# Kernel optimization log

Measured on AMD Instinct MI355X. Metric: run time of the kernel, lower is better.

The kernel has to match this reference:

```python
import jax, jax.numpy as jnp
import numpy as np

N = 50000
E = 600000
F_IN = 128      # float features (in_channels - 1)
CE = 8          # cell embedding dim
D_IN = F_IN + CE  # 136
C = 128         # out_channels
NUM_CELLS = 854
NEG_SLOPE = 0.2
LN_EPS = 1e-5


def _gat_layer(x, src, dst, W, a_src, a_dst, b):
    """PyG GATConv, heads=1, concat=False, add_self_loops already in src/dst.
    x: [N, Din]; src/dst: [Etot]; W: [Din, C]; a_src/a_dst: [C]; b: [C].
    """
    h = x @ W                               # [N, C]
    alpha_src = h @ a_src                   # [N]
    alpha_dst = h @ a_dst                   # [N]
    e = jax.nn.leaky_relu(alpha_src[src] + alpha_dst[dst], NEG_SLOPE)  # [Etot]
    # segment softmax over edges sharing a destination node
    m = jax.ops.segment_max(e, dst, num_segments=N)    # [N] (every node has a self-loop)
    ex = jnp.exp(e - m[dst])                           # [Etot]
    denom = jax.ops.segment_sum(ex, dst, num_segments=N)  # [N]
    alpha = ex / denom[dst]                            # [Etot]
    out = jax.ops.segment_sum(h[src] * alpha[:, None], dst, num_segments=N)  # [N, C]
    return out + b


def _layer_norm(x, g, b):
    mu = jnp.mean(x, axis=-1, keepdims=True)
    var = jnp.var(x, axis=-1, keepdims=True)
    return (x - mu) * jax.lax.rsqrt(var + LN_EPS) * g + b


def setup_inputs() -> dict:
    key = jax.random.key(0)
    ks = jax.random.split(key, 12)
    x_base = jax.random.normal(ks[0], (N, F_IN), dtype=jnp.float32)
    cell_ids = jax.random.randint(ks[1], (N,), 0, NUM_CELLS, dtype=jnp.int64)
    edge_index = jax.random.randint(ks[2], (2, E), 0, N, dtype=jnp.int64)
    s = 0.05
    cell_emb = jax.random.normal(ks[3], (NUM_CELLS, CE), dtype=jnp.float32)
    W1 = jax.random.normal(ks[4], (D_IN, C), dtype=jnp.float32) * s
    a_src1 = jax.random.normal(ks[5], (C,), dtype=jnp.float32) * s
    a_dst1 = jax.random.normal(ks[6], (C,), dtype=jnp.float32) * s
    b1 = jnp.zeros((C,), dtype=jnp.float32)
    ln_g = jnp.ones((C,), dtype=jnp.float32)
    ln_b = jnp.zeros((C,), dtype=jnp.float32)
    W2 = jax.random.normal(ks[7], (C, C), dtype=jnp.float32) * s
    a_src2 = jax.random.normal(ks[8], (C,), dtype=jnp.float32) * s
    a_dst2 = jax.random.normal(ks[9], (C,), dtype=jnp.float32) * s
    b2 = jnp.zeros((C,), dtype=jnp.float32)
    return {
        "x_base": x_base, "cell_ids": cell_ids, "edge_index": edge_index,
        "cell_emb": cell_emb,
        "W1": W1, "a_src1": a_src1, "a_dst1": a_dst1, "b1": b1,
        "ln_g": ln_g, "ln_b": ln_b,
        "W2": W2, "a_src2": a_src2, "a_dst2": a_dst2, "b2": b2,
    }


def reference(x_base, cell_ids, edge_index, cell_emb,
              W1, a_src1, a_dst1, b1, ln_g, ln_b,
              W2, a_src2, a_dst2, b2):
    # embed cell ids and concat (equiv. to x[:, :-1] + Embedding(x[:, -1]))
    x = jnp.concatenate([x_base, cell_emb[cell_ids]], axis=1)   # [N, 136]
    # PyG GATConv adds self-loops internally
    loops = jnp.arange(N, dtype=edge_index.dtype)
    src = jnp.concatenate([edge_index[0], loops])
    dst = jnp.concatenate([edge_index[1], loops])
    # layer 1 + LN + ELU (dropout inactive in eval mode)
    x = _gat_layer(x, src, dst, W1, a_src1, a_dst1, b1)
    x = jax.nn.elu(_layer_norm(x, ln_g, ln_b))
    # layer 2 (no norm/activation on last layer)
    x = _gat_layer(x, src, dst, W2, a_src2, a_dst2, b2)
    return x
```

## Files before the change

### kernel.cpp

```cpp
#include <hip/hip_runtime.h>
#include <hip/hip_fp16.h>
#include <cstdint>
#include <cstddef>

#define NEG_SLOPE 0.2f
#define LN_EPS 1e-5f

constexpr int BS = 256;
constexpr int STRIDE = 96;

typedef _Float16 f16x8 __attribute__((ext_vector_type(8)));
typedef float f32x4 __attribute__((ext_vector_type(4)));

__global__ void k_build(
    const int* __restrict__ esrc, const int* __restrict__ edst,
    int* __restrict__ cnt, int* __restrict__ sn,
    const float* __restrict__ x, const int* __restrict__ cid,
    const float* __restrict__ emb, _Float16* __restrict__ xb,
    const float* __restrict__ W1, const float* __restrict__ W2,
    _Float16* __restrict__ Wt1, _Float16* __restrict__ Wt2,
    int e, int etot, int n, int npad, int nbE, int xblocks)
{
    int b = blockIdx.x;
    if (b < nbE) {
        int i = b * BS + threadIdx.x;
        if (i >= etot) return;
        int s, d;
        if (i < e) { s = esrc[i]; d = edst[i]; }
        else       { s = d = i - e; }
        int slot = atomicAdd(&cnt[d], 1);
        if (slot < STRIDE)
            sn[d * STRIDE + slot] = s << 8;
    } else if (b < nbE + xblocks) {
        int r = (b - nbE) * 8 + (threadIdx.x >> 5);
        int c = threadIdx.x & 31;
        if (r >= npad) return;
        _Float16* row = xb + (size_t)r * 160;
        if (r < n) {
            const float* xr = x + (size_t)r * 128;
            #pragma unroll
            for (int k = 0; k < 4; ++k) row[c + 32 * k] = (_Float16)xr[c + 32 * k];
            float v = (c < 8) ? emb[cid[r] * 8 + c] : 0.f;
            row[128 + c] = (_Float16)v;
        } else {
            #pragma unroll
            for (int k = 0; k < 5; ++k) row[c + 32 * k] = (_Float16)0.f;
        }
    } else {
        int idx = (b - nbE - xblocks) * BS + threadIdx.x;
        if (idx < 128 * 160) {
            int nn = idx / 160, k = idx - nn * 160;
            Wt1[idx] = (_Float16)((k < 136) ? W1[(size_t)k * 128 + nn] : 0.f);
        } else if (idx < 128 * 160 + 128 * 128) {
            int j = idx - 128 * 160;
            int nn = j >> 7, k = j & 127;
            Wt2[j] = (_Float16)W2[(size_t)k * 128 + nn];
        }
    }
}

template<int KP>
__global__ __launch_bounds__(64) void k_gemm_mfma(
    const _Float16* __restrict__ A, const _Float16* __restrict__ Bt,
    const float* __restrict__ a_src, const float* __restrict__ a_dst,
    _Float16* __restrict__ hb, float* __restrict__ as_,
    float* __restrict__ ad_, int n)
{
    int lane = threadIdx.x;
    int r15 = lane & 15, q = lane >> 4;
    int rowBase = blockIdx.x * 64;

    f32x4 acc[8][4] = {};

    const _Float16* Wp[8];
    #pragma unroll
    for (int s = 0; s < 8; ++s)
        Wp[s] = Bt + (size_t)(s * 16 + r15) * KP + q * 8;
    const _Float16* Xp[4];
    #pragma unroll
    for (int t = 0; t < 4; ++t)
        Xp[t] = A + (size_t)(rowBase + t * 16 + r15) * KP + q * 8;

    #pragma unroll
    for (int k0 = 0; k0 < KP; k0 += 32) {
        f16x8 wv[8], xv[4];
        #pragma unroll
        for (int s = 0; s < 8; ++s) wv[s] = *(const f16x8*)(Wp[s] + k0);
        #pragma unroll
        for (int t = 0; t < 4; ++t) xv[t] = *(const f16x8*)(Xp[t] + k0);
        #pragma unroll
        for (int s = 0; s < 8; ++s)
            #pragma unroll
            for (int t = 0; t < 4; ++t)
                acc[s][t] = __builtin_amdgcn_mfma_f32_16x16x32_f16(wv[s], xv[t], acc[s][t], 0, 0, 0);
    }

    float4 asv[8], adv[8];
    #pragma unroll
    for (int s = 0; s < 8; ++s) {
        asv[s] = *(const float4*)&a_src[s * 16 + q * 4];
        adv[s] = *(const float4*)&a_dst[s * 16 + q * 4];
    }

    #pragma unroll
    for (int t = 0; t < 4; ++t) {
        int row = rowBase + t * 16 + r15;
        bool ok = row < n;
        float vs = 0.f, vd = 0.f;
        #pragma unroll
        for (int s = 0; s < 8; ++s) {
            f32x4 d = acc[s][t];
            vs += d[0]*asv[s].x + d[1]*asv[s].y + d[2]*asv[s].z + d[3]*asv[s].w;
            vd += d[0]*adv[s].x + d[1]*adv[s].y + d[2]*adv[s].z + d[3]*adv[s].w;
            if (ok) {
                ushort4 u;
                u.x = __half_as_ushort(__float2half_rn(d[0]));
                u.y = __half_as_ushort(__float2half_rn(d[1]));
                u.z = __half_as_ushort(__float2half_rn(d[2]));
                u.w = __half_as_ushort(__float2half_rn(d[3]));
                *(ushort4*)&hb[(size_t)row * 128 + s * 16 + q * 4] = u;
            }
        }
        vs += __shfl_xor(vs, 16); vs += __shfl_xor(vs, 32);
        vd += __shfl_xor(vd, 16); vd += __shfl_xor(vd, 32);
        if (ok && q == 0) { as_[row] = vs; ad_[row] = vd; }
    }
}

template<bool LN_ELU, bool OUT_HALF>
__global__ __launch_bounds__(256) void k_agg(
    const _Float16* __restrict__ hb, const int* __restrict__ sn,
    const int* __restrict__ cnt, const float* __restrict__ as_,
    const float* __restrict__ ad_, const float* __restrict__ bias,
    const float* __restrict__ ln_g, const float* __restrict__ ln_b,
    void* __restrict__ outv, int n_nodes)
{
    int wave = threadIdx.x >> 6, lane = threadIdx.x & 63;
    int n = blockIdx.x * 4 + wave;
    if (n >= n_nodes) return;
    int len = cnt[n];
    len = len < STRIDE ? len : STRIDE;
    len = __builtin_amdgcn_readfirstlane(len);
    int start = n * STRIDE;
    int l4 = lane & 15, q = lane >> 4;
    float adv = ad_[n];
    const char* hbB = (const char*)hb;

    float acc[8] = {0.f, 0.f, 0.f, 0.f, 0.f, 0.f, 0.f, 0.f};
    float dsum = 0.f;
    for (int j = 0; j < len; j += 16) {
        int rem = len - j;
        int offB = (l4 < rem) ? sn[start + j + l4] : 0;
        float t = as_[offB >> 8] + adv;
        t = t > 0.f ? t : NEG_SLOPE * t;
        float w0 = __expf(fminf(t, 70.f));
        #pragma unroll
        for (int v = 0; v < 4; ++v) {
            int e = 4 * v + q;
            int ob  = __shfl(offB, e);
            float w = __shfl(w0, e);
            if (e < rem) {
                f16x8 hv = *(const f16x8*)(hbB + ob + l4 * 16);
                #pragma unroll
                for (int c = 0; c < 8; ++c)
                    acc[c] = fmaf(w, (float)hv[c], acc[c]);
                dsum += w;
            }
        }
    }
    #pragma unroll
    for (int c = 0; c < 8; ++c) {
        acc[c] += __shfl_xor(acc[c], 16);
        acc[c] += __shfl_xor(acc[c], 32);
    }
    dsum += __shfl_xor(dsum, 16);
    dsum += __shfl_xor(dsum, 32);

    float inv = 1.f / dsum;
    float4 b0 = *(const float4*)&bias[l4 * 8];
    float4 b1 = *(const float4*)&bias[l4 * 8 + 4];
    float vv[8];
    vv[0] = acc[0] * inv + b0.x; vv[1] = acc[1] * inv + b0.y;
    vv[2] = acc[2] * inv + b0.z; vv[3] = acc[3] * inv + b0.w;
    vv[4] = acc[4] * inv + b1.x; vv[5] = acc[5] * inv + b1.y;
    vv[6] = acc[6] * inv + b1.z; vv[7] = acc[7] * inv + b1.w;

    if (LN_ELU) {
        float s1 = 0.f, s2 = 0.f;
        #pragma unroll
        for (int c = 0; c < 8; ++c) { s1 += vv[c]; s2 += vv[c] * vv[c]; }
        #pragma unroll
        for (int o = 1; o < 16; o <<= 1) {
            s1 += __shfl_xor(s1, o);
            s2 += __shfl_xor(s2, o);
        }
        float mean = s1 * (1.f / 128.f);
        float var  = s2 * (1.f / 128.f) - mean * mean;
        float r = rsqrtf(var + LN_EPS);
        float4 g0 = *(const float4*)&ln_g[l4 * 8];
        float4 g1 = *(const float4*)&ln_g[l4 * 8 + 4];
        float4 p0 = *(const float4*)&ln_b[l4 * 8];
        float4 p1 = *(const float4*)&ln_b[l4 * 8 + 4];
        float gg[8] = {g0.x, g0.y, g0.z, g0.w, g1.x, g1.y, g1.z, g1.w};
        float pp[8] = {p0.x, p0.y, p0.z, p0.w, p1.x, p1.y, p1.z, p1.w};
        #pragma unroll
        for (int c = 0; c < 8; ++c) {
            float t = (vv[c] - mean) * r * gg[c] + pp[c];
            vv[c] = t > 0.f ? t : __expf(t) - 1.f;
        }
    }

    if (q == 0) {
        if (OUT_HALF) {
            _Float16* out = (_Float16*)outv;
            f16x8 o;
            #pragma unroll
            for (int c = 0; c < 8; ++c) o[c] = (_Float16)vv[c];
            *(f16x8*)(out + (size_t)n * 128 + l4 * 8) = o;
        } else {
            float* out = (float*)outv;
            float4 o0 = make_float4(vv[0], vv[1], vv[2], vv[3]);
            float4 o1 = make_float4(vv[4], vv[5], vv[6], vv[7]);
            *(float4*)(out + (size_t)n * 128 + l4 * 8)     = o0;
            *(float4*)(out + (size_t)n * 128 + l4 * 8 + 4) = o1;
        }
    }
}


extern "C" void kernel_launch(void* const* d_in, const int* in_sizes, int n_in,
                              void* d_out, int out_size, void* d_ws, size_t ws_size,
                              hipStream_t stream) {
    const float* x_base   = (const float*)d_in[0];
    const int*   cell_ids = (const int*)d_in[1];
    const int*   eidx     = (const int*)d_in[2];
    const float* cell_emb = (const float*)d_in[3];
    const float* W1     = (const float*)d_in[4];
    const float* a_src1 = (const float*)d_in[5];
    const float* a_dst1 = (const float*)d_in[6];
    const float* b1     = (const float*)d_in[7];
    const float* ln_g   = (const float*)d_in[8];
    const float* ln_b   = (const float*)d_in[9];
    const float* W2     = (const float*)d_in[10];
    const float* a_src2 = (const float*)d_in[11];
    const float* a_dst2 = (const float*)d_in[12];
    const float* b2     = (const float*)d_in[13];

    const int N = in_sizes[0] / 128;
    const int E = in_sizes[2] / 2;
    const int ETOT = E + N;
    const int gridG = (N + 63) / 64;
    const int Npad  = gridG * 64;

    const int* esrc = eidx;
    const int* edst = eidx + E;

    auto align = [](size_t v) { return (v + 255) & ~(size_t)255; };
    char* p = (char*)d_ws;
    int*   cnt    = (int*)p;   p += align((size_t)N * 4);
    int*   sn     = (int*)p;   p += align((size_t)N * STRIDE * 4);
    _Float16* xb  = (_Float16*)p; p += align((size_t)Npad * 160 * 2);
    _Float16* yb  = (_Float16*)p; p += align((size_t)Npad * 128 * 2);
    _Float16* hb  = (_Float16*)p; p += align((size_t)N * 128 * 2);
    _Float16* Wt1 = (_Float16*)p; p += align((size_t)128 * 160 * 2);
    _Float16* Wt2 = (_Float16*)p; p += align((size_t)128 * 128 * 2);
    float* as_    = (float*)p; p += align((size_t)N * 4);
    float* ad_    = (float*)p; p += align((size_t)N * 4);
    (void)ws_size; (void)n_in; (void)out_size;

    const int nbE = (ETOT + BS - 1) / BS;
    const int xblocks = (Npad + 7) / 8;
    const int wblocks = (128 * 160 + 128 * 128 + BS - 1) / BS;

    hipMemsetAsync(cnt, 0, (size_t)N * 4, stream);
    k_build<<<nbE + xblocks + wblocks, BS, 0, stream>>>(
        esrc, edst, cnt, sn,
        x_base, cell_ids, cell_emb, xb, W1, W2, Wt1, Wt2,
        E, ETOT, N, Npad, nbE, xblocks);

    k_gemm_mfma<160><<<gridG, 64, 0, stream>>>(xb, Wt1, a_src1, a_dst1, hb, as_, ad_, N);
    k_agg<true, true><<<(N + 3) / 4, 256, 0, stream>>>(
        hb, sn, cnt, as_, ad_, b1, ln_g, ln_b, (void*)yb, N);

    k_gemm_mfma<128><<<gridG, 64, 0, stream>>>(yb, Wt2, a_src2, a_dst2, hb, as_, ad_, N);
    k_agg<false, false><<<(N + 3) / 4, 256, 0, stream>>>(
        hb, sn, cnt, as_, ad_, b2, ln_g, ln_b, d_out, N);
}
```

Measured before the change: 239.3 us.

## Build compact CSR adjacency via count, scan, and placement instead of fixed-stride slots

Replaces the fixed 96-slot per-node neighbor buffer with a compact CSR layout. The build kernel now only counts in-degrees, a block scan with a global atomic computes each node's offset, and a placement kernel scatters source indices into the compact array. This removes the degree cap and the mostly empty padded buffer, so the aggregation kernels read denser neighbor lists. It adds two extra kernel launches and a second pass of atomics over all edges. Because node ranges are assigned through atomics, their order in memory is nondeterministic.

```diff
diff --git a/kernel.cpp b/kernel.cpp
--- a/kernel.cpp
+++ b/kernel.cpp
@@ -7,14 +7,13 @@
 #define LN_EPS 1e-5f
 
 constexpr int BS = 256;
-constexpr int STRIDE = 96;
 
 typedef _Float16 f16x8 __attribute__((ext_vector_type(8)));
 typedef float f32x4 __attribute__((ext_vector_type(4)));
 
 __global__ void k_build(
-    const int* __restrict__ esrc, const int* __restrict__ edst,
-    int* __restrict__ cnt, int* __restrict__ sn,
+    const int* __restrict__ edst,
+    int* __restrict__ cnt,
     const float* __restrict__ x, const int* __restrict__ cid,
     const float* __restrict__ emb, _Float16* __restrict__ xb,
     const float* __restrict__ W1, const float* __restrict__ W2,
@@ -25,12 +24,8 @@
     if (b < nbE) {
         int i = b * BS + threadIdx.x;
         if (i >= etot) return;
-        int s, d;
-        if (i < e) { s = esrc[i]; d = edst[i]; }
-        else       { s = d = i - e; }
-        int slot = atomicAdd(&cnt[d], 1);
-        if (slot < STRIDE)
-            sn[d * STRIDE + slot] = s << 8;
+        int d = (i < e) ? edst[i] : i - e;
+        atomicAdd(&cnt[d], 1);
     } else if (b < nbE + xblocks) {
         int r = (b - nbE) * 8 + (threadIdx.x >> 5);
         int c = threadIdx.x & 31;
@@ -59,6 +54,43 @@
     }
 }
 
+__global__ void k_scan(const int* __restrict__ cnt, int* __restrict__ gctr,
+                       int* __restrict__ offs, int* __restrict__ wptr, int n)
+{
+    __shared__ int sm[BS];
+    __shared__ int base;
+    int i = blockIdx.x * BS + threadIdx.x;
+    int len = (i < n) ? cnt[i] : 0;
+    sm[threadIdx.x] = len;
+    __syncthreads();
+    for (int o = 1; o < BS; o <<= 1) {
+        int t = (threadIdx.x >= o) ? sm[threadIdx.x - o] : 0;
+        __syncthreads();
+        sm[threadIdx.x] += t;
+        __syncthreads();
+    }
+    if (threadIdx.x == BS - 1) base = atomicAdd(gctr, sm[BS - 1]);
+    __syncthreads();
+    if (i < n) {
+        int st = base + sm[threadIdx.x] - len;
+        offs[i] = st;
+        wptr[i] = st;
+    }
+}
+
+__global__ void k_place(const int* __restrict__ esrc, const int* __restrict__ edst,
+                        int* __restrict__ wptr, int* __restrict__ sn,
+                        int e, int etot)
+{
+    int i = blockIdx.x * BS + threadIdx.x;
+    if (i >= etot) return;
+    int s, d;
+    if (i < e) { s = esrc[i]; d = edst[i]; }
+    else       { s = d = i - e; }
+    int pos = atomicAdd(&wptr[d], 1);
+    sn[pos] = s << 8;
+}
+
 template<int KP>
 __global__ __launch_bounds__(64) void k_gemm_mfma(
     const _Float16* __restrict__ A, const _Float16* __restrict__ Bt,
@@ -130,7 +162,8 @@
 template<bool LN_ELU, bool OUT_HALF>
 __global__ __launch_bounds__(256) void k_agg(
     const _Float16* __restrict__ hb, const int* __restrict__ sn,
-    const int* __restrict__ cnt, const float* __restrict__ as_,
+    const int* __restrict__ offs, const int* __restrict__ cnt,
+    const float* __restrict__ as_,
     const float* __restrict__ ad_, const float* __restrict__ bias,
     const float* __restrict__ ln_g, const float* __restrict__ ln_b,
     void* __restrict__ outv, int n_nodes)
@@ -138,10 +171,8 @@
     int wave = threadIdx.x >> 6, lane = threadIdx.x & 63;
     int n = blockIdx.x * 4 + wave;
     if (n >= n_nodes) return;
-    int len = cnt[n];
-    len = len < STRIDE ? len : STRIDE;
-    len = __builtin_amdgcn_readfirstlane(len);
-    int start = n * STRIDE;
+    int start = __builtin_amdgcn_readfirstlane(offs[n]);
+    int len   = __builtin_amdgcn_readfirstlane(cnt[n]);
     int l4 = lane & 15, q = lane >> 4;
     float adv = ad_[n];
     const char* hbB = (const char*)hb;
@@ -258,7 +289,10 @@
     auto align = [](size_t v) { return (v + 255) & ~(size_t)255; };
     char* p = (char*)d_ws;
     int*   cnt    = (int*)p;   p += align((size_t)N * 4);
-    int*   sn     = (int*)p;   p += align((size_t)N * STRIDE * 4);
+    int*   gctr   = (int*)p;   p += align(256);
+    int*   offs   = (int*)p;   p += align((size_t)N * 4);
+    int*   wptr   = (int*)p;   p += align((size_t)N * 4);
+    int*   sn     = (int*)p;   p += align((size_t)(ETOT + 16) * 4);
     _Float16* xb  = (_Float16*)p; p += align((size_t)Npad * 160 * 2);
     _Float16* yb  = (_Float16*)p; p += align((size_t)Npad * 128 * 2);
     _Float16* hb  = (_Float16*)p; p += align((size_t)N * 128 * 2);
@@ -268,21 +302,24 @@
     float* ad_    = (float*)p; p += align((size_t)N * 4);
     (void)ws_size; (void)n_in; (void)out_size;
 
+    const int nbN = (N + BS - 1) / BS;
     const int nbE = (ETOT + BS - 1) / BS;
     const int xblocks = (Npad + 7) / 8;
     const int wblocks = (128 * 160 + 128 * 128 + BS - 1) / BS;
 
-    hipMemsetAsync(cnt, 0, (size_t)N * 4, stream);
+    hipMemsetAsync(cnt, 0, align((size_t)N * 4) + 256, stream);
     k_build<<<nbE + xblocks + wblocks, BS, 0, stream>>>(
-        esrc, edst, cnt, sn,
+        edst, cnt,
         x_base, cell_ids, cell_emb, xb, W1, W2, Wt1, Wt2,
         E, ETOT, N, Npad, nbE, xblocks);
+    k_scan<<<nbN, BS, 0, stream>>>(cnt, gctr, offs, wptr, N);
+    k_place<<<nbE, BS, 0, stream>>>(esrc, edst, wptr, sn, E, ETOT);
 
     k_gemm_mfma<160><<<gridG, 64, 0, stream>>>(xb, Wt1, a_src1, a_dst1, hb, as_, ad_, N);
     k_agg<true, true><<<(N + 3) / 4, 256, 0, stream>>>(
-        hb, sn, cnt, as_, ad_, b1, ln_g, ln_b, (void*)yb, N);
+        hb, sn, offs, cnt, as_, ad_, b1, ln_g, ln_b, (void*)yb, N);
 
     k_gemm_mfma<128><<<gridG, 64, 0, stream>>>(yb, Wt2, a_src2, a_dst2, hb, as_, ad_, N);
     k_agg<false, false><<<(N + 3) / 4, 256, 0, stream>>>(
-        hb, sn, cnt, as_, ad_, b2, ln_g, ln_b, d_out, N);
-}
+        hb, sn, offs, cnt, as_, ad_, b2, ln_g, ln_b, d_out, N);
+}
```

New measurement: 265.1 us. 10.8% more time.

## Split GEMM tile across four waves and store neighbor lists as 16-bit indices

Applied to the files above, without the earlier changes.

The MFMA GEMM now runs 256-thread blocks covering 32 rows, with each wave computing a 16x64 output tile instead of one wave computing 64x128. Attention-score partial dot products are combined through shared memory. This cuts per-wave accumulator registers and raises the number of waves in flight. Separately, neighbor source indices are stored as unsigned short instead of pre-shifted int, halving adjacency memory traffic; this relies on N fitting in 16 bits (50000 < 65536).

```diff
diff --git a/kernel.cpp b/kernel.cpp
--- a/kernel.cpp
+++ b/kernel.cpp
@@ -14,7 +14,7 @@
 
 __global__ void k_build(
     const int* __restrict__ esrc, const int* __restrict__ edst,
-    int* __restrict__ cnt, int* __restrict__ sn,
+    int* __restrict__ cnt, unsigned short* __restrict__ sn,
     const float* __restrict__ x, const int* __restrict__ cid,
     const float* __restrict__ emb, _Float16* __restrict__ xb,
     const float* __restrict__ W1, const float* __restrict__ W2,
@@ -30,7 +30,7 @@
         else       { s = d = i - e; }
         int slot = atomicAdd(&cnt[d], 1);
         if (slot < STRIDE)
-            sn[d * STRIDE + slot] = s << 8;
+            sn[d * STRIDE + slot] = (unsigned short)s;
     } else if (b < nbE + xblocks) {
         int r = (b - nbE) * 8 + (threadIdx.x >> 5);
         int c = threadIdx.x & 31;
@@ -60,76 +60,71 @@
 }
 
 template<int KP>
-__global__ __launch_bounds__(64) void k_gemm_mfma(
+__global__ __launch_bounds__(256) void k_gemm_mfma(
     const _Float16* __restrict__ A, const _Float16* __restrict__ Bt,
     const float* __restrict__ a_src, const float* __restrict__ a_dst,
     _Float16* __restrict__ hb, float* __restrict__ as_,
     float* __restrict__ ad_, int n)
 {
-    int lane = threadIdx.x;
+    __shared__ float red[2][16][2][2];
+    int tid = threadIdx.x;
+    int wave = tid >> 6, lane = tid & 63;
+    int rg = wave >> 1, ch = wave & 1;
     int r15 = lane & 15, q = lane >> 4;
-    int rowBase = blockIdx.x * 64;
-
-    f32x4 acc[8][4] = {};
-
-    const _Float16* Wp[8];
-    #pragma unroll
-    for (int s = 0; s < 8; ++s)
-        Wp[s] = Bt + (size_t)(s * 16 + r15) * KP + q * 8;
-    const _Float16* Xp[4];
-    #pragma unroll
-    for (int t = 0; t < 4; ++t)
-        Xp[t] = A + (size_t)(rowBase + t * 16 + r15) * KP + q * 8;
+    int rowBase = blockIdx.x * 32 + rg * 16;
+    int colBase = ch * 64;
+
+    f32x4 acc[4] = {};
+
+    const _Float16* Wp[4];
+    #pragma unroll
+    for (int s = 0; s < 4; ++s)
+        Wp[s] = Bt + (size_t)(colBase + s * 16 + r15) * KP + q * 8;
+    const _Float16* Xp = A + (size_t)(rowBase + r15) * KP + q * 8;
 
     #pragma unroll
     for (int k0 = 0; k0 < KP; k0 += 32) {
-        f16x8 wv[8], xv[4];
-        #pragma unroll
-        for (int s = 0; s < 8; ++s) wv[s] = *(const f16x8*)(Wp[s] + k0);
-        #pragma unroll
-        for (int t = 0; t < 4; ++t) xv[t] = *(const f16x8*)(Xp[t] + k0);
-        #pragma unroll
-        for (int s = 0; s < 8; ++s)
-            #pragma unroll
-            for (int t = 0; t < 4; ++t)
-                acc[s][t] = __builtin_amdgcn_mfma_f32_16x16x32_f16(wv[s], xv[t], acc[s][t], 0, 0, 0);
-    }
-
-    float4 asv[8], adv[8];
-    #pragma unroll
-    for (int s = 0; s < 8; ++s) {
-        asv[s] = *(const float4*)&a_src[s * 16 + q * 4];
-        adv[s] = *(const float4*)&a_dst[s * 16 + q * 4];
-    }
-
-    #pragma unroll
-    for (int t = 0; t < 4; ++t) {
-        int row = rowBase + t * 16 + r15;
-        bool ok = row < n;
-        float vs = 0.f, vd = 0.f;
-        #pragma unroll
-        for (int s = 0; s < 8; ++s) {
-            f32x4 d = acc[s][t];
-            vs += d[0]*asv[s].x + d[1]*asv[s].y + d[2]*asv[s].z + d[3]*asv[s].w;
-            vd += d[0]*adv[s].x + d[1]*adv[s].y + d[2]*adv[s].z + d[3]*adv[s].w;
-            if (ok) {
-                ushort4 u;
-                u.x = __half_as_ushort(__float2half_rn(d[0]));
-                u.y = __half_as_ushort(__float2half_rn(d[1]));
-                u.z = __half_as_ushort(__float2half_rn(d[2]));
-                u.w = __half_as_ushort(__float2half_rn(d[3]));
-                *(ushort4*)&hb[(size_t)row * 128 + s * 16 + q * 4] = u;
-            }
-        }
-        vs += __shfl_xor(vs, 16); vs += __shfl_xor(vs, 32);
-        vd += __shfl_xor(vd, 16); vd += __shfl_xor(vd, 32);
-        if (ok && q == 0) { as_[row] = vs; ad_[row] = vd; }
+        f16x8 wv[4];
+        #pragma unroll
+        for (int s = 0; s < 4; ++s) wv[s] = *(const f16x8*)(Wp[s] + k0);
+        f16x8 xv = *(const f16x8*)(Xp + k0);
+        #pragma unroll
+        for (int s = 0; s < 4; ++s)
+            acc[s] = __builtin_amdgcn_mfma_f32_16x16x32_f16(wv[s], xv, acc[s], 0, 0, 0);
+    }
+
+    int row = rowBase + r15;
+    bool ok = row < n;
+    float vs = 0.f, vd = 0.f;
+    #pragma unroll
+    for (int s = 0; s < 4; ++s) {
+        float4 as4 = *(const float4*)&a_src[colBase + s * 16 + q * 4];
+        float4 ad4 = *(const float4*)&a_dst[colBase + s * 16 + q * 4];
+        f32x4 d = acc[s];
+        vs += d[0]*as4.x + d[1]*as4.y + d[2]*as4.z + d[3]*as4.w;
+        vd += d[0]*ad4.x + d[1]*ad4.y + d[2]*ad4.z + d[3]*ad4.w;
+        if (ok) {
+            ushort4 u;
+            u.x = __half_as_ushort(__float2half_rn(d[0]));
+            u.y = __half_as_ushort(__float2half_rn(d[1]));
+            u.z = __half_as_ushort(__float2half_rn(d[2]));
+            u.w = __half_as_ushort(__float2half_rn(d[3]));
+            *(ushort4*)&hb[(size_t)row * 128 + colBase + s * 16 + q * 4] = u;
+        }
+    }
+    vs += __shfl_xor(vs, 16); vs += __shfl_xor(vs, 32);
+    vd += __shfl_xor(vd, 16); vd += __shfl_xor(vd, 32);
+    if (q == 0) { red[rg][r15][ch][0] = vs; red[rg][r15][ch][1] = vd; }
+    __syncthreads();
+    if (ch == 0 && q == 0 && ok) {
+        as_[row] = red[rg][r15][0][0] + red[rg][r15][1][0];
+        ad_[row] = red[rg][r15][0][1] + red[rg][r15][1][1];
     }
 }
 
 template<bool LN_ELU, bool OUT_HALF>
 __global__ __launch_bounds__(256) void k_agg(
-    const _Float16* __restrict__ hb, const int* __restrict__ sn,
+    const _Float16* __restrict__ hb, const unsigned short* __restrict__ sn,
     const int* __restrict__ cnt, const float* __restrict__ as_,
     const float* __restrict__ ad_, const float* __restrict__ bias,
     const float* __restrict__ ln_g, const float* __restrict__ ln_b,
@@ -150,7 +145,7 @@
     float dsum = 0.f;
     for (int j = 0; j < len; j += 16) {
         int rem = len - j;
-        int offB = (l4 < rem) ? sn[start + j + l4] : 0;
+        int offB = (l4 < rem) ? ((int)sn[start + j + l4] << 8) : 0;
         float t = as_[offB >> 8] + adv;
         t = t > 0.f ? t : NEG_SLOPE * t;
         float w0 = __expf(fminf(t, 70.f));
@@ -249,8 +244,8 @@
     const int N = in_sizes[0] / 128;
     const int E = in_sizes[2] / 2;
     const int ETOT = E + N;
-    const int gridG = (N + 63) / 64;
-    const int Npad  = gridG * 64;
+    const int Npad  = ((N + 63) / 64) * 64;
+    const int gridG = (N + 31) / 32;
 
     const int* esrc = eidx;
     const int* edst = eidx + E;
@@ -258,7 +253,7 @@
     auto align = [](size_t v) { return (v + 255) & ~(size_t)255; };
     char* p = (char*)d_ws;
     int*   cnt    = (int*)p;   p += align((size_t)N * 4);
-    int*   sn     = (int*)p;   p += align((size_t)N * STRIDE * 4);
+    unsigned short* sn = (unsigned short*)p; p += align((size_t)N * STRIDE * 2 + 64);
     _Float16* xb  = (_Float16*)p; p += align((size_t)Npad * 160 * 2);
     _Float16* yb  = (_Float16*)p; p += align((size_t)Npad * 128 * 2);
     _Float16* hb  = (_Float16*)p; p += align((size_t)N * 128 * 2);
@@ -278,11 +273,11 @@
         x_base, cell_ids, cell_emb, xb, W1, W2, Wt1, Wt2,
         E, ETOT, N, Npad, nbE, xblocks);
 
-    k_gemm_mfma<160><<<gridG, 64, 0, stream>>>(xb, Wt1, a_src1, a_dst1, hb, as_, ad_, N);
+    k_gemm_mfma<160><<<gridG, 256, 0, stream>>>(xb, Wt1, a_src1, a_dst1, hb, as_, ad_, N);
     k_agg<true, true><<<(N + 3) / 4, 256, 0, stream>>>(
         hb, sn, cnt, as_, ad_, b1, ln_g, ln_b, (void*)yb, N);
 
-    k_gemm_mfma<128><<<gridG, 64, 0, stream>>>(yb, Wt2, a_src2, a_dst2, hb, as_, ad_, N);
+    k_gemm_mfma<128><<<gridG, 256, 0, stream>>>(yb, Wt2, a_src2, a_dst2, hb, as_, ad_, N);
     k_agg<false, false><<<(N + 3) / 4, 256, 0, stream>>>(
         hb, sn, cnt, as_, ad_, b2, ln_g, ln_b, d_out, N);
 }
```

Result: slower. 244.1 us (+2.0%).
